# Performance work log

Measured on AMD Instinct MI355X. Metric: run time of the kernel, lower is better.

The kernel has to match this reference:

```python
import jax, jax.numpy as jnp
import numpy as np

NVEC = [100000, 100000, 100000]
OFFSETS = np.concatenate([[0], np.cumsum(NVEC)[:-1]]).astype(np.int32)  # [0,100000,200000]
DIM = 64
B = 500000
HID = 50
IN_DIM = len(NVEC) * DIM + 1  # 193


def setup_inputs() -> dict:
    key = jax.random.key(0)
    ks = jax.random.split(key, 7)
    batch_ind = jax.random.randint(ks[0], (B, len(NVEC)), 0, NVEC[0], dtype=jnp.int32)
    batch_t = jax.random.uniform(ks[1], (B,), dtype=jnp.float32)
    U = jax.random.uniform(ks[2], (int(np.sum(NVEC)), DIM), dtype=jnp.float32)
    W1 = jax.random.normal(ks[3], (IN_DIM, HID), dtype=jnp.float32) * 0.1
    b1 = jax.random.normal(ks[4], (HID,), dtype=jnp.float32) * 0.1
    W2 = jax.random.normal(ks[5], (HID, 1), dtype=jnp.float32) * 0.1
    b2 = jax.random.normal(ks[6], (1,), dtype=jnp.float32) * 0.1
    return {"batch_ind": batch_ind, "batch_t": batch_t, "U": U,
            "W1": W1, "b1": b1, "W2": W2, "b2": b2}


def reference(batch_ind, batch_t, U, W1, b1, W2, b2):
    # per-mode gather: offset each mode's index into the concatenated U table
    offs = jnp.asarray(OFFSETS)  # [nmod]
    idx = batch_ind + offs[None, :]          # [B, nmod] global row ids
    emb = U[idx]                              # [B, nmod, D] single fused gather
    X = jnp.concatenate([emb.reshape(emb.shape[0], -1),
                         batch_t[:, None]], axis=1)  # [B, nmod*D+1]
    h = jnp.tanh(X @ W1 + b1)                 # [B, 50]
    return h @ W2 + b2                        # [B, 1]
```

## Files before the change

### kernel.cpp

```cpp
#include <hip/hip_runtime.h>
#include <hip/hip_bf16.h>

using bf16x8 = __attribute__((ext_vector_type(8))) short;
using f16x8  = __attribute__((ext_vector_type(8))) _Float16;
using f16x4  = __attribute__((ext_vector_type(4))) _Float16;
using f32x4  = __attribute__((ext_vector_type(4))) float;

#define THREADS   256
#define NROWS_U   300000
#define WS_NEED   (NROWS_U * 64 * 2)
#define TPM       6250
#define BPM       521
#define NB_PC     (BPM * 3)
#define NB_MAIN   2048
#define NITERS_M  15625

__device__ __forceinline__ short f2bf(float f) {
    __hip_bfloat16 h = __float2bfloat16(f);
    return __builtin_bit_cast(short, h);
}

__device__ __forceinline__ bf16x8 cvt8(float4 a, float4 b) {
    bf16x8 r;
    r[0] = f2bf(a.x); r[1] = f2bf(a.y); r[2] = f2bf(a.z); r[3] = f2bf(a.w);
    r[4] = f2bf(b.x); r[5] = f2bf(b.y); r[6] = f2bf(b.z); r[7] = f2bf(b.w);
    return r;
}

__global__ __launch_bounds__(THREADS, 8) void pc_kernel(
    const float* __restrict__ U,
    const float* __restrict__ W1,
    _Float16*    __restrict__ V)
{
    const int lane = threadIdx.x & 63;
    const int g    = lane >> 4;
    const int ncol = lane & 15;
    const int warp = threadIdx.x >> 6;
    const int mode = blockIdx.x / BPM;
    const int bloc = blockIdx.x - mode * BPM;

    bf16x8 Bf[8];
    {
        const float* Wm = W1 + mode * 64 * 50;
#pragma unroll
        for (int nt = 0; nt < 4; ++nt) {
            const int n = nt * 16 + ncol;
            const bool vld = n < 50;
#pragma unroll
            for (int ks = 0; ks < 2; ++ks) {
                bf16x8 v;
#pragma unroll
                for (int j = 0; j < 8; ++j) {
                    float w = vld ? Wm[(ks * 32 + g * 8 + j) * 50 + n] : 0.f;
                    v[j] = f2bf(w);
                }
                Bf[nt * 2 + ks] = v;
            }
        }
    }

#pragma unroll 1
    for (int j = 0; j < 3; ++j) {
        int tl = bloc * 12 + warp * 3 + j;
        if (tl > TPM - 1) tl = TPM - 1;
        const int tile = mode * TPM + tl;

        const float* p = U + (size_t)(tile * 16 + ncol) * 64 + g * 8;
        float4 a0 = ((const float4*)p)[0],        a1 = ((const float4*)p)[1];
        float4 a2 = ((const float4*)(p + 32))[0], a3 = ((const float4*)(p + 32))[1];
        bf16x8 A0 = cvt8(a0, a1);
        bf16x8 A1 = cvt8(a2, a3);

        f32x4 acc[4];
#pragma unroll
        for (int nt = 0; nt < 4; ++nt) acc[nt] = (f32x4){0.f, 0.f, 0.f, 0.f};
#pragma unroll
        for (int nt = 0; nt < 4; ++nt) {
            acc[nt] = __builtin_amdgcn_mfma_f32_16x16x32_bf16(A0, Bf[nt * 2 + 0], acc[nt], 0, 0, 0);
            acc[nt] = __builtin_amdgcn_mfma_f32_16x16x32_bf16(A1, Bf[nt * 2 + 1], acc[nt], 0, 0, 0);
        }

        const int base = tile * 16;
#pragma unroll
        for (int r = 0; r < 4; ++r) {
            f16x4 pk;
#pragma unroll
            for (int nt = 0; nt < 4; ++nt) pk[nt] = (_Float16)acc[nt][r];
            *(f16x4*)(V + (size_t)(base + g * 4 + r) * 64 + ncol * 4) = pk;
        }
    }
}

__global__ __launch_bounds__(THREADS) void etl_main(
    const int*      __restrict__ bi,
    const float*    __restrict__ t,
    const _Float16* __restrict__ V,
    const float*    __restrict__ W1,
    const float*    __restrict__ b1,
    const float*    __restrict__ W2,
    const float*    __restrict__ b2,
    float*          __restrict__ out)
{
    const int lane = threadIdx.x & 63;
    const int r8   = lane >> 3;
    const int c    = lane & 7;

    float w192r[8], b1r[8], w2r[8];
#pragma unroll
    for (int j = 0; j < 8; ++j) {
        int pos = c * 8 + j;
        int n = (pos & 3) * 16 + (pos >> 2);
        bool vld = n < 50;
        w192r[j] = vld ? W1[192 * 50 + n] : 0.f;
        b1r[j]   = vld ? b1[n] : 0.f;
        w2r[j]   = vld ? W2[n] : 0.f;
    }
    const float b2v = b2[0];

    const int nwaves = NB_MAIN * (THREADS / 64);
    for (int it = blockIdx.x * (THREADS / 64) + (threadIdx.x >> 6);
         it < NITERS_M; it += nwaves) {
        const int base = it * 32;

        int id[4][3];
#pragma unroll
        for (int u = 0; u < 4; ++u) {
            int r = base + u * 8 + r8;
#pragma unroll
            for (int m = 0; m < 3; ++m)
                id[u][m] = bi[r * 3 + m] + m * 100000;
        }

        f16x8 va[4][3];
#pragma unroll
        for (int u = 0; u < 4; ++u)
#pragma unroll
            for (int m = 0; m < 3; ++m)
                va[u][m] = *(const f16x8*)(V + (size_t)id[u][m] * 64 + c * 8);

        float tv[4];
#pragma unroll
        for (int u = 0; u < 4; ++u) tv[u] = t[base + u * 8 + r8];

#pragma unroll
        for (int u = 0; u < 4; ++u) {
            float acc = 0.f;
#pragma unroll
            for (int j = 0; j < 8; ++j) {
                float h = (float)va[u][0][j] + (float)va[u][1][j] +
                          (float)va[u][2][j] + tv[u] * w192r[j] + b1r[j];
                float e = __expf(2.f * h);
                acc += (1.f - 2.f * __builtin_amdgcn_rcpf(e + 1.f)) * w2r[j];
            }
            acc += __shfl_xor(acc, 1, 64);
            acc += __shfl_xor(acc, 2, 64);
            acc += __shfl_xor(acc, 4, 64);
            if (c == 0) out[base + u * 8 + r8] = acc + b2v;
        }
    }
}

__global__ __launch_bounds__(THREADS) void etl_f32(
    const int*   __restrict__ bi,
    const float* __restrict__ t,
    const float* __restrict__ U,
    const float* __restrict__ W1,
    const float* __restrict__ b1,
    const float* __restrict__ W2,
    const float* __restrict__ b2,
    float*       __restrict__ out)
{
    __shared__ short bsh[24][64][8];
    for (int e = threadIdx.x; e < 24 * 64; e += THREADS) {
        int f = e >> 6, l = e & 63;
        int nt = f / 6, ks = f - nt * 6;
        int n  = nt * 16 + (l & 15);
        int k0 = ks * 32 + ((l >> 4) << 3);
        bf16x8 v;
#pragma unroll
        for (int j = 0; j < 8; ++j) {
            float w = (n < 50) ? W1[(k0 + j) * 50 + n] : 0.f;
            v[j] = f2bf(w);
        }
        *(bf16x8*)(&bsh[f][l][0]) = v;
    }
    __syncthreads();

    const int lane = threadIdx.x & 63;
    const int g    = lane >> 4;
    const int ncol = lane & 15;

    bf16x8 Bf[24];
#pragma unroll
    for (int f = 0; f < 24; ++f) Bf[f] = *(const bf16x8*)(&bsh[f][lane][0]);

    float w192[4], b1r[4], w2r[4];
#pragma unroll
    for (int nt = 0; nt < 4; ++nt) {
        int n = nt * 16 + ncol;
        bool vld = (n < 50);
        w192[nt] = vld ? W1[192 * 50 + n] : 0.f;
        b1r[nt]  = vld ? b1[n] : 0.f;
        w2r[nt]  = vld ? W2[n] : 0.f;
    }
    const float b2v = b2[0];

    const int nwaves = 768 * (THREADS / 64);
    const int wid    = blockIdx.x * (THREADS / 64) + (threadIdx.x >> 6);

    for (int tile = wid; tile < 31250; tile += nwaves) {
        const int base = tile * 16;
        const int row  = base + ncol;
        int i0 = bi[row * 3 + 0];
        int i1 = bi[row * 3 + 1] + 100000;
        int i2 = bi[row * 3 + 2] + 200000;

        bf16x8 A[6];
        const float* p0 = U + (size_t)i0 * 64 + g * 8;
        const float* p1 = U + (size_t)i1 * 64 + g * 8;
        const float* p2 = U + (size_t)i2 * 64 + g * 8;
        A[0] = cvt8(((const float4*)p0)[0], ((const float4*)p0)[1]);
        A[1] = cvt8(((const float4*)(p0 + 32))[0], ((const float4*)(p0 + 32))[1]);
        A[2] = cvt8(((const float4*)p1)[0], ((const float4*)p1)[1]);
        A[3] = cvt8(((const float4*)(p1 + 32))[0], ((const float4*)(p1 + 32))[1]);
        A[4] = cvt8(((const float4*)p2)[0], ((const float4*)p2)[1]);
        A[5] = cvt8(((const float4*)(p2 + 32))[0], ((const float4*)(p2 + 32))[1]);

        f32x4 acc[4];
#pragma unroll
        for (int nt = 0; nt < 4; ++nt) acc[nt] = (f32x4){0.f, 0.f, 0.f, 0.f};
#pragma unroll
        for (int ks = 0; ks < 6; ++ks) {
#pragma unroll
            for (int nt = 0; nt < 4; ++nt) {
                acc[nt] = __builtin_amdgcn_mfma_f32_16x16x32_bf16(
                    A[ks], Bf[nt * 6 + ks], acc[nt], 0, 0, 0);
            }
        }

        float4 tv = *(const float4*)(t + base + g * 4);
        float tarr[4] = {tv.x, tv.y, tv.z, tv.w};
        float part[4] = {0.f, 0.f, 0.f, 0.f};
#pragma unroll
        for (int nt = 0; nt < 4; ++nt) {
#pragma unroll
            for (int r = 0; r < 4; ++r) {
                float pre = acc[nt][r] + tarr[r] * w192[nt] + b1r[nt];
                float e  = __expf(2.f * pre);
                float h  = 1.f - 2.f * __builtin_amdgcn_rcpf(e + 1.f);
                part[r] += h * w2r[nt];
            }
        }
#pragma unroll
        for (int r = 0; r < 4; ++r) {
#pragma unroll
            for (int m = 1; m < 16; m <<= 1)
                part[r] += __shfl_xor(part[r], m, 64);
        }
        if (ncol == 0) {
            float4 o = make_float4(part[0] + b2v, part[1] + b2v,
                                   part[2] + b2v, part[3] + b2v);
            *(float4*)(out + base + g * 4) = o;
        }
    }
}

extern "C" void kernel_launch(void* const* d_in, const int* in_sizes, int n_in,
                              void* d_out, int out_size, void* d_ws, size_t ws_size,
                              hipStream_t stream) {
    const int*   bi = (const int*)  d_in[0];
    const float* t  = (const float*)d_in[1];
    const float* U  = (const float*)d_in[2];
    const float* W1 = (const float*)d_in[3];
    const float* b1 = (const float*)d_in[4];
    const float* W2 = (const float*)d_in[5];
    const float* b2 = (const float*)d_in[6];
    float* out = (float*)d_out;

    if (ws_size >= (size_t)WS_NEED) {
        _Float16* V = (_Float16*)d_ws;
        pc_kernel<<<NB_PC, THREADS, 0, stream>>>(U, W1, V);
        etl_main<<<NB_MAIN, THREADS, 0, stream>>>(bi, t, V, W1, b1, W2, b2, out);
    } else {
        etl_f32<<<768, THREADS, 0, stream>>>(bi, t, U, W1, b1, W2, b2, out);
    }
}
```

Measured before the change: 65.04 us.

## Double-buffer U tile loads into LDS via async global_load_lds in precompute kernel

The precompute kernel now stages each warp's 16-row U tile into shared memory with asynchronous global-to-LDS loads (XOR-swizzled), double-buffered so the next tile's load overlaps the current tile's MFMA work. Each warp handles four tiles instead of three, so fewer blocks are launched, and the occupancy hint drops to 6. The aim is to hide global memory latency in the per-row projection step. The cost is extra LDS usage and hand-managed vmcnt waits that are fragile if the compiler reorders memory operations.

```diff
diff --git a/kernel.cpp b/kernel.cpp
--- a/kernel.cpp
+++ b/kernel.cpp
@@ -10,7 +10,8 @@
 #define NROWS_U   300000
 #define WS_NEED   (NROWS_U * 64 * 2)
 #define TPM       6250
-#define BPM       521
+#define TPB       16
+#define BPM       391
 #define NB_PC     (BPM * 3)
 #define NB_MAIN   2048
 #define NITERS_M  15625
@@ -27,17 +28,48 @@
     return r;
 }
 
-__global__ __launch_bounds__(THREADS, 8) void pc_kernel(
+__device__ __forceinline__ float4 tof4(f32x4 v) {
+    return make_float4(v[0], v[1], v[2], v[3]);
+}
+
+__global__ __launch_bounds__(THREADS, 6) void pc_kernel(
     const float* __restrict__ U,
     const float* __restrict__ W1,
     _Float16*    __restrict__ V)
 {
+    __shared__ __align__(16) float gb[4][2][1024];
+
     const int lane = threadIdx.x & 63;
     const int g    = lane >> 4;
     const int ncol = lane & 15;
     const int warp = threadIdx.x >> 6;
     const int mode = blockIdx.x / BPM;
-    const int bloc = blockIdx.x - mode * BPM;
+    const int bloc = blockIdx.x % BPM;
+
+    const int srow = lane >> 4;
+    const int schk = lane & 15;
+
+    auto tileof = [&](int j) {
+        int tl = bloc * TPB + warp * 4 + j;
+        if (tl > TPM - 1) tl = TPM - 1;
+        return mode * TPM + tl;
+    };
+
+    auto stage = [&](int j, int b) {
+        const int tile = tileof(j);
+#pragma unroll
+        for (int q = 0; q < 4; ++q) {
+            const int row = q * 4 + srow;
+            const float* gp = U + (size_t)(tile * 16 + row) * 64 + ((schk ^ row) << 2);
+            __builtin_amdgcn_global_load_lds(
+                (const __attribute__((address_space(1))) void*)gp,
+                (__attribute__((address_space(3))) void*)(&gb[warp][b][q * 256]),
+                16, 0, 0);
+        }
+    };
+
+    stage(0, 0);
+    stage(1, 1);
 
     bf16x8 Bf[8];
     {
@@ -50,45 +82,55 @@
             for (int ks = 0; ks < 2; ++ks) {
                 bf16x8 v;
 #pragma unroll
-                for (int j = 0; j < 8; ++j) {
-                    float w = vld ? Wm[(ks * 32 + g * 8 + j) * 50 + n] : 0.f;
-                    v[j] = f2bf(w);
+                for (int jj = 0; jj < 8; ++jj) {
+                    float w = vld ? Wm[(ks * 32 + g * 8 + jj) * 50 + n] : 0.f;
+                    v[jj] = f2bf(w);
                 }
                 Bf[nt * 2 + ks] = v;
             }
         }
     }
 
-#pragma unroll 1
-    for (int j = 0; j < 3; ++j) {
-        int tl = bloc * 12 + warp * 3 + j;
-        if (tl > TPM - 1) tl = TPM - 1;
-        const int tile = mode * TPM + tl;
-
-        const float* p = U + (size_t)(tile * 16 + ncol) * 64 + g * 8;
-        float4 a0 = ((const float4*)p)[0],        a1 = ((const float4*)p)[1];
-        float4 a2 = ((const float4*)(p + 32))[0], a3 = ((const float4*)(p + 32))[1];
-        bf16x8 A0 = cvt8(a0, a1);
-        bf16x8 A1 = cvt8(a2, a3);
-
-        f32x4 acc[4];
-#pragma unroll
-        for (int nt = 0; nt < 4; ++nt) acc[nt] = (f32x4){0.f, 0.f, 0.f, 0.f};
-#pragma unroll
-        for (int nt = 0; nt < 4; ++nt) {
-            acc[nt] = __builtin_amdgcn_mfma_f32_16x16x32_bf16(A0, Bf[nt * 2 + 0], acc[nt], 0, 0, 0);
-            acc[nt] = __builtin_amdgcn_mfma_f32_16x16x32_bf16(A1, Bf[nt * 2 + 1], acc[nt], 0, 0, 0);
-        }
-
-        const int base = tile * 16;
-#pragma unroll
-        for (int r = 0; r < 4; ++r) {
-            f16x4 pk;
-#pragma unroll
-            for (int nt = 0; nt < 4; ++nt) pk[nt] = (_Float16)acc[nt][r];
-            *(f16x4*)(V + (size_t)(base + g * 4 + r) * 64 + ncol * 4) = pk;
-        }
-    }
+    const f32x4* lb0 = (const f32x4*)&gb[warp][0][0];
+    const f32x4* lb1 = (const f32x4*)&gb[warp][1][0];
+
+#define PC_BODY(J, B, VMLIT, DO_STAGE)                                         \
+    {                                                                          \
+        asm volatile("s_waitcnt vmcnt(" #VMLIT ")" ::: "memory");              \
+        __builtin_amdgcn_sched_barrier(0);                                     \
+        const f32x4* lb = (B) ? lb1 : lb0;                                     \
+        f32x4 d0 = lb[ncol * 16 + ((2 * g)     ^ ncol)];                       \
+        f32x4 d1 = lb[ncol * 16 + ((2 * g + 1) ^ ncol)];                       \
+        f32x4 d2 = lb[ncol * 16 + ((8 + 2 * g) ^ ncol)];                       \
+        f32x4 d3 = lb[ncol * 16 + ((9 + 2 * g) ^ ncol)];                       \
+        asm volatile("s_waitcnt lgkmcnt(0)" ::: "memory");                     \
+        __builtin_amdgcn_sched_barrier(0);                                     \
+        if (DO_STAGE) stage((J) + 2, B);                                       \
+        bf16x8 A0 = cvt8(tof4(d0), tof4(d1));                                  \
+        bf16x8 A1 = cvt8(tof4(d2), tof4(d3));                                  \
+        f32x4 acc[4];                                                          \
+        _Pragma("unroll")                                                      \
+        for (int nt = 0; nt < 4; ++nt) acc[nt] = (f32x4){0.f, 0.f, 0.f, 0.f};  \
+        _Pragma("unroll")                                                      \
+        for (int nt = 0; nt < 4; ++nt) {                                       \
+            acc[nt] = __builtin_amdgcn_mfma_f32_16x16x32_bf16(A0, Bf[nt*2+0], acc[nt], 0, 0, 0); \
+            acc[nt] = __builtin_amdgcn_mfma_f32_16x16x32_bf16(A1, Bf[nt*2+1], acc[nt], 0, 0, 0); \
+        }                                                                      \
+        const int base = tileof(J) * 16;                                       \
+        _Pragma("unroll")                                                      \
+        for (int r = 0; r < 4; ++r) {                                          \
+            f16x4 pk;                                                          \
+            _Pragma("unroll")                                                  \
+            for (int nt = 0; nt < 4; ++nt) pk[nt] = (_Float16)acc[nt][r];      \
+            *(f16x4*)(V + (size_t)(base + g * 4 + r) * 64 + ncol * 4) = pk;    \
+        }                                                                      \
+    }
+
+    PC_BODY(0, 0, 4,  true)
+    PC_BODY(1, 1, 8,  true)
+    PC_BODY(2, 0, 12, false)
+    PC_BODY(3, 1, 8,  false)
+#undef PC_BODY
 }
 
 __global__ __launch_bounds__(THREADS) void etl_main(
```

Measured after the change: 55.75 us, median of 2. 14.3% less time.
